# Optimization experiments

Measured on AMD Instinct MI355X. Metric: run time of the kernel, lower is better.

The kernel has to match this reference:

```python
import jax, jax.numpy as jnp
import numpy as np

N, C_IN, D, K, C_OUT = 50000, 256, 25000, 16, 256


def setup_inputs() -> dict:
    key = jax.random.key(0)
    k1, k2, k3, k4 = jax.random.split(key, 4)
    x = jax.random.normal(k1, (N, C_IN), dtype=jnp.float32)
    symm_norm = jax.random.uniform(k2, (N,), dtype=jnp.float32)
    domains = jax.random.randint(k3, (D, K), 0, N, dtype=jnp.int64)
    # Linear params: in = 2*C_IN (order-1 transfer doubles channels), xavier-uniform
    fan_in, fan_out = 2 * C_IN, C_OUT
    limit = float(np.sqrt(6.0 / (fan_in + fan_out)))
    w = jax.random.uniform(k4, (2 * C_IN, C_OUT), dtype=jnp.float32,
                           minval=-limit, maxval=limit)
    b = jnp.zeros((C_OUT,), dtype=jnp.float32)
    return {"x": x, "symm_norm": symm_norm, "domains": domains, "w": w, "b": b}


def reference(x, symm_norm, domains, w, b):
    # symmetric normalization: outer(features, symm_norm) -> per-node scale
    xs = x * symm_norm[:, None]                      # [N, C]
    # transfer1 (ptensors1 over singleton domains -> ptensors1 over target domains):
    # gather node features into each target domain; the two order-1 linmaps
    # (identity, broadcast-of-sum over the singleton intersection) coincide.
    g = jnp.take(xs, domains, axis=0)                # [D, K, C]
    f = jnp.concatenate([g, g], axis=-1)             # [D, K, 2C]
    # linear projection
    y = jnp.einsum('dkc,co->dko', f, w) + b          # [D, K, C_OUT]
    return y
```

## Files before the change

### kernel.cpp

```cpp
#include <hip/hip_runtime.h>


#define GM 50000
#define GK 256
#define GN 256
#define RTOT 400000
#define BM 128
#define BN 128
#define BK 16
#define LDA (BM + 4)
#define LDB (BN + 4)
#define CAP 64
#define OVF_MAX 4096

typedef float v4f __attribute__((ext_vector_type(4)));

__global__ __launch_bounds__(256)
void zero_kernel(int* __restrict__ cnt, int* __restrict__ ovf_cnt) {
    const int i = blockIdx.x * 256 + threadIdx.x;
    if (i < GM) cnt[i] = 0;
    if (i == 0) *ovf_cnt = 0;
}

__global__ __launch_bounds__(256)
void build_kernel(const int* __restrict__ dm, int* __restrict__ cnt,
                  int* __restrict__ bucket, int* __restrict__ ovf,
                  int* __restrict__ ovf_cnt) {
    const int r = blockIdx.x * 256 + threadIdx.x;
    if (r >= RTOT) return;
    const int n = dm[r];
    const int slot = atomicAdd(&cnt[n], 1);
    if (slot < CAP) {
        bucket[n * CAP + slot] = r;
    } else {
        const int o = atomicAdd(ovf_cnt, 1);
        if (o < OVF_MAX) ovf[o] = r;
    }
}

__global__ __launch_bounds__(256, 4)
void gemm_scatter_kernel(const float* __restrict__ x,
                         const float* __restrict__ sn,
                         const float* __restrict__ w,
                         const float* __restrict__ b,
                         const int* __restrict__ cnt,
                         const int* __restrict__ bucket,
                         float* __restrict__ out,
                         float* __restrict__ z) {
    __shared__ float As[BK][LDA];
    __shared__ float Bs[BK][LDB];

    const int t  = threadIdx.x;
    const int tx = t & 15;
    const int ty = t >> 4;
    const int rowBase = blockIdx.x * BM;
    const int colBase = blockIdx.y * BN;

    const int a_m = t >> 2;
    const int a_k = (t & 3) * 4;
    const int b_k = t >> 5;
    const int b_n = (t & 31) * 4;

    float acc[8][8] = {};

    for (int k0 = 0; k0 < GK; k0 += BK) {
        #pragma unroll
        for (int h = 0; h < 2; ++h) {
            const int mr = a_m + h * 64;
            const int m  = rowBase + mr;
            float4 v = make_float4(0.f, 0.f, 0.f, 0.f);
            if (m < GM) {
                v = *reinterpret_cast<const float4*>(&x[(size_t)m * GK + k0 + a_k]);
                const float s = sn[m];
                v.x *= s; v.y *= s; v.z *= s; v.w *= s;
            }
            As[a_k + 0][mr] = v.x;
            As[a_k + 1][mr] = v.y;
            As[a_k + 2][mr] = v.z;
            As[a_k + 3][mr] = v.w;
        }
        #pragma unroll
        for (int h = 0; h < 2; ++h) {
            const int kk = b_k + h * 8;
            const int gk = k0 + kk;
            const int gn = colBase + b_n;
            float4 v0 = *reinterpret_cast<const float4*>(&w[(size_t)gk * GN + gn]);
            float4 v1 = *reinterpret_cast<const float4*>(&w[(size_t)(gk + 256) * GN + gn]);
            v0.x += v1.x; v0.y += v1.y; v0.z += v1.z; v0.w += v1.w;
            *reinterpret_cast<float4*>(&Bs[kk][b_n]) = v0;
        }
        __syncthreads();

        #pragma unroll
        for (int kk = 0; kk < BK; ++kk) {
            float a[8], bb[8];
            *reinterpret_cast<float4*>(&a[0])  =
                *reinterpret_cast<const float4*>(&As[kk][ty * 4]);
            *reinterpret_cast<float4*>(&a[4])  =
                *reinterpret_cast<const float4*>(&As[kk][64 + ty * 4]);
            *reinterpret_cast<float4*>(&bb[0]) =
                *reinterpret_cast<const float4*>(&Bs[kk][tx * 4]);
            *reinterpret_cast<float4*>(&bb[4]) =
                *reinterpret_cast<const float4*>(&Bs[kk][64 + tx * 4]);
            #pragma unroll
            for (int i = 0; i < 8; ++i)
                #pragma unroll
                for (int j = 0; j < 8; ++j)
                    acc[i][j] += a[i] * bb[j];
        }
        __syncthreads();
    }

    const int n0 = colBase + tx * 4;
    const float4 bias0 = *reinterpret_cast<const float4*>(&b[n0]);
    const float4 bias1 = *reinterpret_cast<const float4*>(&b[n0 + 64]);
    #pragma unroll
    for (int i = 0; i < 8; ++i) {
        const int m = rowBase + (i >> 2) * 64 + ty * 4 + (i & 3);
        if (m >= GM) continue;
        v4f v0, v1;
        v0.x = acc[i][0] + bias0.x; v0.y = acc[i][1] + bias0.y;
        v0.z = acc[i][2] + bias0.z; v0.w = acc[i][3] + bias0.w;
        v1.x = acc[i][4] + bias1.x; v1.y = acc[i][5] + bias1.y;
        v1.z = acc[i][6] + bias1.z; v1.w = acc[i][7] + bias1.w;
        const int c  = cnt[m];
        const int cc = c < CAP ? c : CAP;
        const int* bk = &bucket[m * CAP];
        for (int j = 0; j < cc; ++j) {
            const int r = bk[j];
            float* orow = &out[(size_t)r * GN];
            __builtin_nontemporal_store(v0, reinterpret_cast<v4f*>(&orow[n0]));
            __builtin_nontemporal_store(v1, reinterpret_cast<v4f*>(&orow[n0 + 64]));
        }
        if (c > CAP) {
            float* zr = &z[(size_t)m * GN];
            *reinterpret_cast<v4f*>(&zr[n0])      = v0;
            *reinterpret_cast<v4f*>(&zr[n0 + 64]) = v1;
        }
    }
}

__global__ __launch_bounds__(256)
void cleanup_kernel(const float* __restrict__ z, const int* __restrict__ dm,
                    const int* __restrict__ ovf, const int* __restrict__ ovf_cnt,
                    float* __restrict__ out) {
    int nov = *ovf_cnt;
    if (nov > OVF_MAX) nov = OVF_MAX;
    const int lane = threadIdx.x & 63;
    const int wid  = (blockIdx.x * 256 + threadIdx.x) >> 6;
    const int nw   = (gridDim.x * 256) >> 6;
    for (int i = wid; i < nov; i += nw) {
        const int r = ovf[i];
        const int n = dm[r];
        const float4 v = *reinterpret_cast<const float4*>(&z[(size_t)n * GN + lane * 4]);
        *reinterpret_cast<float4*>(&out[(size_t)r * GN + lane * 4]) = v;
    }
}

extern "C" void kernel_launch(void* const* d_in, const int* in_sizes, int n_in,
                              void* d_out, int out_size, void* d_ws, size_t ws_size,
                              hipStream_t stream) {
    const float* x  = (const float*)d_in[0];
    const float* sn = (const float*)d_in[1];
    const int*   dm = (const int*)d_in[2];
    const float* w  = (const float*)d_in[3];
    const float* b  = (const float*)d_in[4];
    float* out = (float*)d_out;

    char* ws = (char*)d_ws;
    float* z      = (float*)ws;
    int*   cnt    = (int*)(ws + 51200000);
    int*   bucket = cnt + GM;
    int*   ovf_cnt= bucket + (size_t)GM * CAP;
    int*   ovf    = ovf_cnt + 4;

    zero_kernel<<<(GM + 255) / 256, 256, 0, stream>>>(cnt, ovf_cnt);
    build_kernel<<<(RTOT + 255) / 256, 256, 0, stream>>>(dm, cnt, bucket, ovf, ovf_cnt);

    dim3 gemm_grid((GM + BM - 1) / BM, GN / BN);
    gemm_scatter_kernel<<<gemm_grid, 256, 0, stream>>>(x, sn, w, b, cnt, bucket, out, z);

    cleanup_kernel<<<64, 256, 0, stream>>>(z, dm, ovf, ovf_cnt, out);
}
```

Measured before the change: 539.7 us.

## Use split-bf16 MFMA for the GEMM with pre-transposed split weights

Replaces the FP32 FMA register-tiled GEMM with bf16 MFMA 16x16x32 instructions, using a hi/lo bf16 split of both activations and weights (three products) to keep near-FP32 accuracy. A new kernel folds the duplicated weight halves, splits them into bf16 hi/lo parts and transposes them. The epilogue now scatters scalar floats per lane instead of float4 vectors. The aim is to cut compute time in the GEMM, at the cost of extra conversion work and narrower stores in the write-bound scatter.

```diff
diff --git a/kernel.cpp b/kernel.cpp
--- a/kernel.cpp
+++ b/kernel.cpp
@@ -7,13 +7,20 @@
 #define RTOT 400000
 #define BM 128
 #define BN 128
-#define BK 16
-#define LDA (BM + 4)
-#define LDB (BN + 4)
+#define BK 32
+#define LDK 40
 #define CAP 64
 #define OVF_MAX 4096
 
-typedef float v4f __attribute__((ext_vector_type(4)));
+using bf16x8 = __attribute__((ext_vector_type(8))) short;
+using f32x4  = __attribute__((ext_vector_type(4))) float;
+
+__device__ inline ushort f2bf(float f) {
+    uint u = __float_as_uint(f);
+    u += 0x7FFFu + ((u >> 16) & 1u);
+    return (ushort)(u >> 16);
+}
+__device__ inline float bf2f(ushort h) { return __uint_as_float(((uint)h) << 16); }
 
 __global__ __launch_bounds__(256)
 void zero_kernel(int* __restrict__ cnt, int* __restrict__ ovf_cnt) {
@@ -38,104 +45,155 @@
     }
 }
 
-__global__ __launch_bounds__(256, 4)
+__global__ __launch_bounds__(256)
+void wsplit_kernel(const float* __restrict__ w, ushort* __restrict__ whT,
+                   ushort* __restrict__ wlT) {
+    const int idx = blockIdx.x * 256 + threadIdx.x;
+    const int k = idx >> 8, n = idx & 255;
+    const float we = w[k * GN + n] + w[(k + 256) * GN + n];
+    const ushort hi = f2bf(we);
+    const ushort lo = f2bf(we - bf2f(hi));
+    whT[n * GK + k] = hi;
+    wlT[n * GK + k] = lo;
+}
+
+__global__ __launch_bounds__(256)
 void gemm_scatter_kernel(const float* __restrict__ x,
                          const float* __restrict__ sn,
-                         const float* __restrict__ w,
+                         const ushort* __restrict__ whT,
+                         const ushort* __restrict__ wlT,
                          const float* __restrict__ b,
                          const int* __restrict__ cnt,
                          const int* __restrict__ bucket,
                          float* __restrict__ out,
                          float* __restrict__ z) {
-    __shared__ float As[BK][LDA];
-    __shared__ float Bs[BK][LDB];
-
-    const int t  = threadIdx.x;
-    const int tx = t & 15;
-    const int ty = t >> 4;
+    __shared__ ushort Ah[BM][LDK];
+    __shared__ ushort Al[BM][LDK];
+    __shared__ ushort Bh[BN][LDK];
+    __shared__ ushort Bl[BN][LDK];
+
+    const int t = threadIdx.x;
     const int rowBase = blockIdx.x * BM;
     const int colBase = blockIdx.y * BN;
 
-    const int a_m = t >> 2;
-    const int a_k = (t & 3) * 4;
-    const int b_k = t >> 5;
-    const int b_n = (t & 31) * 4;
-
-    float acc[8][8] = {};
+    const int srow = t >> 1;
+    const int skh  = (t & 1) * 16;
+
+    const int wid  = t >> 6;
+    const int lane = t & 63;
+    const int fr   = lane & 15;
+    const int fq   = lane >> 4;
+    const int wm   = (wid >> 1) * 64;
+    const int wn   = (wid & 1) * 64;
+
+    f32x4 acc[4][4];
+    #pragma unroll
+    for (int i = 0; i < 4; ++i)
+        #pragma unroll
+        for (int j = 0; j < 4; ++j)
+            acc[i][j] = (f32x4){0.f, 0.f, 0.f, 0.f};
 
     for (int k0 = 0; k0 < GK; k0 += BK) {
-        #pragma unroll
-        for (int h = 0; h < 2; ++h) {
-            const int mr = a_m + h * 64;
-            const int m  = rowBase + mr;
-            float4 v = make_float4(0.f, 0.f, 0.f, 0.f);
+        {
+            const int m = rowBase + srow;
+            float v[16];
             if (m < GM) {
-                v = *reinterpret_cast<const float4*>(&x[(size_t)m * GK + k0 + a_k]);
                 const float s = sn[m];
-                v.x *= s; v.y *= s; v.z *= s; v.w *= s;
-            }
-            As[a_k + 0][mr] = v.x;
-            As[a_k + 1][mr] = v.y;
-            As[a_k + 2][mr] = v.z;
-            As[a_k + 3][mr] = v.w;
-        }
-        #pragma unroll
-        for (int h = 0; h < 2; ++h) {
-            const int kk = b_k + h * 8;
-            const int gk = k0 + kk;
-            const int gn = colBase + b_n;
-            float4 v0 = *reinterpret_cast<const float4*>(&w[(size_t)gk * GN + gn]);
-            float4 v1 = *reinterpret_cast<const float4*>(&w[(size_t)(gk + 256) * GN + gn]);
-            v0.x += v1.x; v0.y += v1.y; v0.z += v1.z; v0.w += v1.w;
-            *reinterpret_cast<float4*>(&Bs[kk][b_n]) = v0;
+                const float4* xp =
+                    reinterpret_cast<const float4*>(&x[(size_t)m * GK + k0 + skh]);
+                #pragma unroll
+                for (int q = 0; q < 4; ++q) {
+                    const float4 f = xp[q];
+                    v[q*4+0] = f.x * s; v[q*4+1] = f.y * s;
+                    v[q*4+2] = f.z * s; v[q*4+3] = f.w * s;
+                }
+            } else {
+                #pragma unroll
+                for (int q = 0; q < 16; ++q) v[q] = 0.f;
+            }
+            union { ushort u[8]; uint4 q4; } h0, h1, l0, l1;
+            #pragma unroll
+            for (int q = 0; q < 8; ++q) {
+                const ushort h = f2bf(v[q]);
+                h0.u[q] = h; l0.u[q] = f2bf(v[q] - bf2f(h));
+            }
+            #pragma unroll
+            for (int q = 0; q < 8; ++q) {
+                const ushort h = f2bf(v[8 + q]);
+                h1.u[q] = h; l1.u[q] = f2bf(v[8 + q] - bf2f(h));
+            }
+            *reinterpret_cast<uint4*>(&Ah[srow][skh])     = h0.q4;
+            *reinterpret_cast<uint4*>(&Ah[srow][skh + 8]) = h1.q4;
+            *reinterpret_cast<uint4*>(&Al[srow][skh])     = l0.q4;
+            *reinterpret_cast<uint4*>(&Al[srow][skh + 8]) = l1.q4;
+        }
+        {
+            const int n = colBase + srow;
+            const uint4* ph =
+                reinterpret_cast<const uint4*>(&whT[(size_t)n * GK + k0 + skh]);
+            const uint4* pl =
+                reinterpret_cast<const uint4*>(&wlT[(size_t)n * GK + k0 + skh]);
+            *reinterpret_cast<uint4*>(&Bh[srow][skh])     = ph[0];
+            *reinterpret_cast<uint4*>(&Bh[srow][skh + 8]) = ph[1];
+            *reinterpret_cast<uint4*>(&Bl[srow][skh])     = pl[0];
+            *reinterpret_cast<uint4*>(&Bl[srow][skh + 8]) = pl[1];
         }
         __syncthreads();
 
-        #pragma unroll
-        for (int kk = 0; kk < BK; ++kk) {
-            float a[8], bb[8];
-            *reinterpret_cast<float4*>(&a[0])  =
-                *reinterpret_cast<const float4*>(&As[kk][ty * 4]);
-            *reinterpret_cast<float4*>(&a[4])  =
-                *reinterpret_cast<const float4*>(&As[kk][64 + ty * 4]);
-            *reinterpret_cast<float4*>(&bb[0]) =
-                *reinterpret_cast<const float4*>(&Bs[kk][tx * 4]);
-            *reinterpret_cast<float4*>(&bb[4]) =
-                *reinterpret_cast<const float4*>(&Bs[kk][64 + tx * 4]);
+        bf16x8 bh[4], bl[4];
+        #pragma unroll
+        for (int ni = 0; ni < 4; ++ni) {
+            const int br = wn + ni * 16 + fr;
+            bh[ni] = *reinterpret_cast<const bf16x8*>(&Bh[br][fq * 8]);
+            bl[ni] = *reinterpret_cast<const bf16x8*>(&Bl[br][fq * 8]);
+        }
+        #pragma unroll
+        for (int mi = 0; mi < 4; ++mi) {
+            const int ar = wm + mi * 16 + fr;
+            const bf16x8 ah = *reinterpret_cast<const bf16x8*>(&Ah[ar][fq * 8]);
+            const bf16x8 al = *reinterpret_cast<const bf16x8*>(&Al[ar][fq * 8]);
             #pragma unroll
-            for (int i = 0; i < 8; ++i)
-                #pragma unroll
-                for (int j = 0; j < 8; ++j)
-                    acc[i][j] += a[i] * bb[j];
+            for (int ni = 0; ni < 4; ++ni) {
+                acc[mi][ni] = __builtin_amdgcn_mfma_f32_16x16x32_bf16(
+                    ah, bh[ni], acc[mi][ni], 0, 0, 0);
+                acc[mi][ni] = __builtin_amdgcn_mfma_f32_16x16x32_bf16(
+                    ah, bl[ni], acc[mi][ni], 0, 0, 0);
+                acc[mi][ni] = __builtin_amdgcn_mfma_f32_16x16x32_bf16(
+                    al, bh[ni], acc[mi][ni], 0, 0, 0);
+            }
         }
         __syncthreads();
     }
 
-    const int n0 = colBase + tx * 4;
-    const float4 bias0 = *reinterpret_cast<const float4*>(&b[n0]);
-    const float4 bias1 = *reinterpret_cast<const float4*>(&b[n0 + 64]);
+    float bias[4];
     #pragma unroll
-    for (int i = 0; i < 8; ++i) {
-        const int m = rowBase + (i >> 2) * 64 + ty * 4 + (i & 3);
-        if (m >= GM) continue;
-        v4f v0, v1;
-        v0.x = acc[i][0] + bias0.x; v0.y = acc[i][1] + bias0.y;
-        v0.z = acc[i][2] + bias0.z; v0.w = acc[i][3] + bias0.w;
-        v1.x = acc[i][4] + bias1.x; v1.y = acc[i][5] + bias1.y;
-        v1.z = acc[i][6] + bias1.z; v1.w = acc[i][7] + bias1.w;
-        const int c  = cnt[m];
-        const int cc = c < CAP ? c : CAP;
-        const int* bk = &bucket[m * CAP];
-        for (int j = 0; j < cc; ++j) {
-            const int r = bk[j];
-            float* orow = &out[(size_t)r * GN];
-            __builtin_nontemporal_store(v0, reinterpret_cast<v4f*>(&orow[n0]));
-            __builtin_nontemporal_store(v1, reinterpret_cast<v4f*>(&orow[n0 + 64]));
-        }
-        if (c > CAP) {
-            float* zr = &z[(size_t)m * GN];
-            *reinterpret_cast<v4f*>(&zr[n0])      = v0;
-            *reinterpret_cast<v4f*>(&zr[n0 + 64]) = v1;
+    for (int ni = 0; ni < 4; ++ni) bias[ni] = b[colBase + wn + ni * 16 + fr];
+
+    const int ncol0 = colBase + wn + fr;
+    #pragma unroll
+    for (int mi = 0; mi < 4; ++mi) {
+        #pragma unroll
+        for (int r = 0; r < 4; ++r) {
+            const int m = rowBase + wm + mi * 16 + fq * 4 + r;
+            if (m >= GM) continue;
+            const float v0 = acc[mi][0][r] + bias[0];
+            const float v1 = acc[mi][1][r] + bias[1];
+            const float v2 = acc[mi][2][r] + bias[2];
+            const float v3 = acc[mi][3][r] + bias[3];
+            const int c  = cnt[m];
+            const int cc = c < CAP ? c : CAP;
+            const int* bk = &bucket[m * CAP];
+            for (int j = 0; j < cc; ++j) {
+                float* orow = &out[(size_t)bk[j] * GN + ncol0];
+                __builtin_nontemporal_store(v0, orow);
+                __builtin_nontemporal_store(v1, orow + 16);
+                __builtin_nontemporal_store(v2, orow + 32);
+                __builtin_nontemporal_store(v3, orow + 48);
+            }
+            if (c > CAP) {
+                float* zr = &z[(size_t)m * GN + ncol0];
+                zr[0] = v0; zr[16] = v1; zr[32] = v2; zr[48] = v3;
+            }
         }
     }
 }
@@ -168,17 +226,21 @@
     float* out = (float*)d_out;
 
     char* ws = (char*)d_ws;
-    float* z      = (float*)ws;
-    int*   cnt    = (int*)(ws + 51200000);
-    int*   bucket = cnt + GM;
-    int*   ovf_cnt= bucket + (size_t)GM * CAP;
-    int*   ovf    = ovf_cnt + 4;
+    float*  z       = (float*)ws;
+    int*    cnt     = (int*)(ws + 51200000);
+    int*    bucket  = cnt + GM;
+    int*    ovf_cnt = bucket + (size_t)GM * CAP;
+    int*    ovf     = ovf_cnt + 4;
+    ushort* whT     = (ushort*)(ovf + OVF_MAX);
+    ushort* wlT     = whT + GK * GN;
 
     zero_kernel<<<(GM + 255) / 256, 256, 0, stream>>>(cnt, ovf_cnt);
     build_kernel<<<(RTOT + 255) / 256, 256, 0, stream>>>(dm, cnt, bucket, ovf, ovf_cnt);
+    wsplit_kernel<<<(GK * GN) / 256, 256, 0, stream>>>(w, whT, wlT);
 
     dim3 gemm_grid((GM + BM - 1) / BM, GN / BN);
-    gemm_scatter_kernel<<<gemm_grid, 256, 0, stream>>>(x, sn, w, b, cnt, bucket, out, z);
+    gemm_scatter_kernel<<<gemm_grid, 256, 0, stream>>>(x, sn, whT, wlT, b,
+                                                       cnt, bucket, out, z);
 
     cleanup_kernel<<<64, 256, 0, stream>>>(z, dm, ovf, ovf_cnt, out);
 }
```

Measured after the change: 553.7 us. 2.6% more time.
